# Performance work log

Hardware: AMD Instinct MI355X
Metric: run time of the kernel (lower is better)

The kernel has to match this reference:

```python
import jax, jax.numpy as jnp
import numpy as np

HEAD_NUM, HEAD_DIM, HIDDEN = 16, 64, 1024


def setup_inputs() -> dict:
    key = jax.random.key(0)
    ks = jax.random.split(key, 9)
    s = 1.0 / np.sqrt(HIDDEN)
    x = jax.random.normal(ks[0], (4, 2048, HIDDEN), dtype=jnp.float32)
    Wq = jax.random.uniform(ks[1], (HIDDEN, HIDDEN), jnp.float32, -s, s)
    bq = jax.random.uniform(ks[2], (HIDDEN,), jnp.float32, -s, s)
    Wk = jax.random.uniform(ks[3], (HIDDEN, HIDDEN), jnp.float32, -s, s)
    bk = jax.random.uniform(ks[4], (HIDDEN,), jnp.float32, -s, s)
    Wv = jax.random.uniform(ks[5], (HIDDEN, HIDDEN), jnp.float32, -s, s)
    bv = jax.random.uniform(ks[6], (HIDDEN,), jnp.float32, -s, s)
    Wo = jax.random.uniform(ks[7], (HIDDEN, HIDDEN), jnp.float32, -s, s)
    bo = jax.random.uniform(ks[8], (HIDDEN,), jnp.float32, -s, s)
    return {"x": x, "Wq": Wq, "bq": bq, "Wk": Wk, "bk": bk,
            "Wv": Wv, "bv": bv, "Wo": Wo, "bo": bo}


def reference(x, Wq, bq, Wk, bk, Wv, bv, Wo, bo):
    B, S, _ = x.shape
    H, D = HEAD_NUM, HEAD_DIM
    # Linear: x @ W^T + b (torch nn.Linear convention)
    q = (x @ Wq.T + bq).reshape(B, S, H, D).transpose(0, 2, 1, 3)  # [B,H,S,D]
    k = (x @ Wk.T + bk).reshape(B, S, H, D).transpose(0, 2, 1, 3)
    v = (x @ Wv.T + bv).reshape(B, S, H, D).transpose(0, 2, 1, 3)
    scores = jnp.einsum('bhqd,bhkd->bhqk', q, k) / np.sqrt(D)  # [B,H,S,S]
    attn = jax.nn.softmax(scores, axis=-1)  # dropout p=0.0 -> identity
    out = jnp.einsum('bhqk,bhkd->bhqd', attn, v)
    out = out.transpose(0, 2, 1, 3).reshape(B, S, H * D)
    return out @ Wo.T + bo
```

## Files before the change

### kernel.cpp

```cpp
#include <hip/hip_runtime.h>
#include <hip/hip_bf16.h>


typedef __attribute__((ext_vector_type(8))) short short8;
typedef __attribute__((ext_vector_type(4))) short short4b;
typedef __attribute__((ext_vector_type(4))) float floatx4;

#define HID 1024
#define SEQ 2048
#define BATCH 4
#define NH 16
#define HD 64
#define M_TOT (BATCH * SEQ)

#define BM 128
#define BN 128
#define BK 64

#define SCALE2 0.1803368801111204f

typedef const __attribute__((address_space(1))) void g_void;
typedef __attribute__((address_space(3))) void lds_void;

static __device__ __forceinline__ ushort f2bf(float f) {
    union { float f; unsigned int u; } v;
    v.f = f;
    unsigned int u = v.u;
    return (ushort)((u + 0x7fffu + ((u >> 16) & 1u)) >> 16);
}
static __device__ __forceinline__ ushort4 f4tobf(float4 f) {
    ushort4 r;
    r.x = f2bf(f.x); r.y = f2bf(f.y); r.z = f2bf(f.z); r.w = f2bf(f.w);
    return r;
}
static __device__ __forceinline__ unsigned int pack2bf_trunc(float lo, float hi) {
    union { float f; unsigned int u; } a, b;
    a.f = lo; b.f = hi;
    return (b.u & 0xffff0000u) | (a.u >> 16);
}

#define X_F4 (M_TOT * HID / 4)
#define W_F4 (HID * HID / 4)

__global__ __launch_bounds__(256) void convert_bf16(
    const float* __restrict__ x,
    const float* __restrict__ wq, const float* __restrict__ wk,
    const float* __restrict__ wv, const float* __restrict__ wo,
    ushort* __restrict__ xo,
    ushort* __restrict__ wqo, ushort* __restrict__ wko,
    ushort* __restrict__ wvo, ushort* __restrict__ woo)
{
    long i = (long)blockIdx.x * 256 + threadIdx.x;
    const float4* src; ushort4* dst; long off;
    if (i < X_F4)                  { src = (const float4*)x;  dst = (ushort4*)xo;  off = i; }
    else if (i < X_F4 + W_F4)      { src = (const float4*)wq; dst = (ushort4*)wqo; off = i - X_F4; }
    else if (i < X_F4 + 2 * W_F4)  { src = (const float4*)wk; dst = (ushort4*)wko; off = i - X_F4 - W_F4; }
    else if (i < X_F4 + 3 * W_F4)  { src = (const float4*)wv; dst = (ushort4*)wvo; off = i - X_F4 - 2 * W_F4; }
    else                           { src = (const float4*)wo; dst = (ushort4*)woo; off = i - X_F4 - 3 * W_F4; }
    dst[off] = f4tobf(src[off]);
}

template <int MODE>
__global__ __launch_bounds__(256) void gemm_bf(
    const ushort* __restrict__ A,
    const ushort* __restrict__ W0, const ushort* __restrict__ W1,
    const ushort* __restrict__ W2,
    const float* __restrict__ b0, const float* __restrict__ b1,
    const float* __restrict__ b2,
    ushort* __restrict__ o0, ushort* __restrict__ o1, ushort* __restrict__ o2,
    float* __restrict__ of)
{
    __shared__ ushort As[BM * BK];
    __shared__ ushort Bs[BN * BK];

    const int tid  = threadIdx.x;
    const int wave = tid >> 6;
    const int lane = tid & 63;
    const int l16  = lane & 15;
    const int lq   = lane >> 4;

    const int m0 = blockIdx.x * BM;
    const int n0 = blockIdx.y * BN;
    const int z  = (MODE == 1) ? blockIdx.z : 0;

    const ushort* W   = (z == 0) ? W0 : (z == 1) ? W1 : W2;
    const float* bias = (z == 0) ? b0 : (z == 1) ? b1 : b2;

    const int wm = (wave & 1) * 64;
    const int wn = (wave >> 1) * 64;

    const int srow = lane >> 3;
    const int schk = (lane & 7) ^ srow;
    const ushort* gA = A + (size_t)(m0 + wave * 32 + srow) * HID + schk * 8;
    const ushort* gW = W + (size_t)(n0 + wave * 32 + srow) * HID + schk * 8;
    ushort* lA = As + (wave * 32) * BK;
    ushort* lB = Bs + (wave * 32) * BK;

    floatx4 acc[4][4];
#pragma unroll
    for (int i = 0; i < 4; i++)
#pragma unroll
        for (int j = 0; j < 4; j++)
            acc[i][j] = (floatx4){0.f, 0.f, 0.f, 0.f};

    for (int k0 = 0; k0 < HID; k0 += BK) {
        __syncthreads();
#pragma unroll
        for (int i = 0; i < 4; i++) {
            __builtin_amdgcn_global_load_lds(
                (g_void*)(gA + (size_t)(8 * i) * HID + k0),
                (lds_void*)(lA + (8 * i) * BK), 16, 0, 0);
            __builtin_amdgcn_global_load_lds(
                (g_void*)(gW + (size_t)(8 * i) * HID + k0),
                (lds_void*)(lB + (8 * i) * BK), 16, 0, 0);
        }
        __syncthreads();

        const int sw = l16 & 7;
#pragma unroll
        for (int kk8 = 0; kk8 < 8; kk8 += 4) {
            short8 a[4], b[4];
#pragma unroll
            for (int i = 0; i < 4; i++)
                a[i] = *(const short8*)(&As[(wm + i * 16 + l16) * BK + ((lq + kk8) ^ sw) * 8]);
#pragma unroll
            for (int j = 0; j < 4; j++)
                b[j] = *(const short8*)(&Bs[(wn + j * 16 + l16) * BK + ((lq + kk8) ^ sw) * 8]);
#pragma unroll
            for (int i = 0; i < 4; i++)
#pragma unroll
                for (int j = 0; j < 4; j++)
                    acc[i][j] = __builtin_amdgcn_mfma_f32_16x16x32_bf16(
                        a[i], b[j], acc[i][j], 0, 0, 0);
        }
    }

    if (MODE == 0) {
#pragma unroll
        for (int j = 0; j < 4; j++) {
            int n = n0 + wn + j * 16 + l16;
            float bv = bias[n];
#pragma unroll
            for (int i = 0; i < 4; i++)
#pragma unroll
                for (int r = 0; r < 4; r++) {
                    int m = m0 + wm + i * 16 + lq * 4 + r;
                    of[(size_t)m * HID + n] = acc[i][j][r] + bv;
                }
        }
    } else if (z == 2) {
        ushort* out = o2;
#pragma unroll
        for (int j = 0; j < 4; j++) {
            int n = n0 + wn + j * 16 + l16;
            float bv = bias[n];
            int h_ = n >> 6, d_ = n & (HD - 1);
#pragma unroll
            for (int i = 0; i < 4; i++) {
                int m = m0 + wm + i * 16 + lq * 4;
                int b_ = m >> 11, s0 = m & (SEQ - 1);
                ushort4 pk;
                pk.x = f2bf(acc[i][j][0] + bv);
                pk.y = f2bf(acc[i][j][1] + bv);
                pk.z = f2bf(acc[i][j][2] + bv);
                pk.w = f2bf(acc[i][j][3] + bv);
                *(ushort4*)(out + (((size_t)b_ * NH + h_) * HD + d_) * SEQ + s0) = pk;
            }
        }
    } else {
        ushort* out = (z == 0) ? o0 : o1;
        const float sc = (z == 0) ? SCALE2 : 1.0f;
#pragma unroll
        for (int j = 0; j < 4; j++) {
            int n = n0 + wn + j * 16 + l16;
            float bv = bias[n];
            int h_ = n >> 6, d_ = n & (HD - 1);
#pragma unroll
            for (int i = 0; i < 4; i++)
#pragma unroll
                for (int r = 0; r < 4; r++) {
                    int m = m0 + wm + i * 16 + lq * 4 + r;
                    int b_ = m >> 11, s_ = m & (SEQ - 1);
                    out[(((size_t)b_ * NH + h_) * SEQ + s_) * HD + d_] =
                        f2bf((acc[i][j][r] + bv) * sc);
                }
        }
    }
}

__global__ __launch_bounds__(256) void attn_flash(
    const ushort* __restrict__ q, const ushort* __restrict__ k,
    const ushort* __restrict__ v, ushort* __restrict__ o)
{
    __shared__ ushort Ks[64 * 64];
    __shared__ ushort Vs[64 * 64];

    const int tid  = threadIdx.x;
    const int wave = tid >> 6;
    const int lane = tid & 63;
    const int l16  = lane & 15;
    const int lq   = lane >> 4;
    const int e    = l16 & 7;

    const int qb = blockIdx.x;
    const int bh = blockIdx.y;
    const int b_ = bh >> 4, h_ = bh & 15;

    const size_t base = (size_t)bh * SEQ * HD;
    const ushort* Q  = q + base;
    const ushort* K  = k + base;
    const ushort* Vt = v + base;

    const int q0 = qb * 128 + wave * 32;

    short8 qf[2][2];
#pragma unroll
    for (int f = 0; f < 2; f++) {
        const ushort* qrow = Q + (size_t)(q0 + f * 16 + l16) * HD;
        qf[f][0] = *(const short8*)(qrow + lq * 8);
        qf[f][1] = *(const short8*)(qrow + 32 + lq * 8);
    }

    const int srow = lane >> 3;
    const int schk = (lane & 7) ^ srow;
    const ushort* gK = K  + (size_t)(wave * 8 + srow) * HD  + schk * 8;
    const ushort* gV = Vt + (size_t)(wave * 8 + srow) * SEQ + schk * 8;

    floatx4 oacc[2][4];
#pragma unroll
    for (int f = 0; f < 2; f++)
#pragma unroll
        for (int jd = 0; jd < 4; jd++) oacc[f][jd] = (floatx4){0.f, 0.f, 0.f, 0.f};
    float l_[2] = {0.f, 0.f};

    const int c0 = lq ^ e;
    const int c1 = (lq + 4) ^ e;

    for (int t = 0; t < SEQ / 64; t++) {
        __syncthreads();
#pragma unroll
        for (int i = 0; i < 2; i++) {
            __builtin_amdgcn_global_load_lds(
                (g_void*)(gK + (size_t)(t * 64 + i * 32) * HD),
                (lds_void*)(Ks + (i * 32 + wave * 8) * 64), 16, 0, 0);
            __builtin_amdgcn_global_load_lds(
                (g_void*)(gV + (size_t)(i * 32) * SEQ + t * 64),
                (lds_void*)(Vs + (i * 32 + wave * 8) * 64), 16, 0, 0);
        }
        __syncthreads();

        floatx4 st[2][4];
#pragma unroll
        for (int j = 0; j < 4; j++) {
            short8 kf0 = *(const short8*)(&Ks[(j * 16 + l16) * 64 + c0 * 8]);
            short8 kf1 = *(const short8*)(&Ks[(j * 16 + l16) * 64 + c1 * 8]);
#pragma unroll
            for (int f = 0; f < 2; f++) {
                floatx4 zz = (floatx4){0.f, 0.f, 0.f, 0.f};
                zz = __builtin_amdgcn_mfma_f32_16x16x32_bf16(kf0, qf[f][0], zz, 0, 0, 0);
                st[f][j] = __builtin_amdgcn_mfma_f32_16x16x32_bf16(kf1, qf[f][1], zz, 0, 0, 0);
            }
        }

        short4b pf[2][4];
#pragma unroll
        for (int f = 0; f < 2; f++) {
            float rs = 0.f;
#pragma unroll
            for (int j = 0; j < 4; j++) {
                float p0 = __builtin_amdgcn_exp2f(st[f][j][0]);
                float p1 = __builtin_amdgcn_exp2f(st[f][j][1]);
                float p2 = __builtin_amdgcn_exp2f(st[f][j][2]);
                float p3 = __builtin_amdgcn_exp2f(st[f][j][3]);
                rs += (p0 + p1) + (p2 + p3);
                union { unsigned int u[2]; short4b s; } pk;
                pk.u[0] = pack2bf_trunc(p0, p1);
                pk.u[1] = pack2bf_trunc(p2, p3);
                pf[f][j] = pk.s;
            }
            l_[f] += rs;
        }

#pragma unroll
        for (int j = 0; j < 4; j++) {
#pragma unroll
            for (int jd = 0; jd < 4; jd++) {
                short4b vf = *(const short4b*)(
                    &Vs[(jd * 16 + l16) * 64 + ((2 * j + (lq >> 1)) ^ e) * 8 + (lq & 1) * 4]);
                oacc[0][jd] = __builtin_amdgcn_mfma_f32_16x16x16bf16_1k(
                    vf, pf[0][j], oacc[0][jd], 0, 0, 0);
                oacc[1][jd] = __builtin_amdgcn_mfma_f32_16x16x16bf16_1k(
                    vf, pf[1][j], oacc[1][jd], 0, 0, 0);
            }
        }
    }

#pragma unroll
    for (int f = 0; f < 2; f++) {
        l_[f] += __shfl_xor(l_[f], 16, 64);
        l_[f] += __shfl_xor(l_[f], 32, 64);
    }
#pragma unroll
    for (int f = 0; f < 2; f++) {
        int qg = q0 + f * 16 + l16;
        float invl = 1.0f / l_[f];
#pragma unroll
        for (int jd = 0; jd < 4; jd++) {
            ushort4 pk;
            pk.x = f2bf(oacc[f][jd][0] * invl);
            pk.y = f2bf(oacc[f][jd][1] * invl);
            pk.z = f2bf(oacc[f][jd][2] * invl);
            pk.w = f2bf(oacc[f][jd][3] * invl);
            *(ushort4*)(o + ((size_t)b_ * SEQ + qg) * HID + h_ * HD + jd * 16 + lq * 4) = pk;
        }
    }
}

extern "C" void kernel_launch(void* const* d_in, const int* in_sizes, int n_in,
                              void* d_out, int out_size, void* d_ws, size_t ws_size,
                              hipStream_t stream)
{
    const float* x  = (const float*)d_in[0];
    const float* Wq = (const float*)d_in[1];
    const float* bq = (const float*)d_in[2];
    const float* Wk = (const float*)d_in[3];
    const float* bk = (const float*)d_in[4];
    const float* Wv = (const float*)d_in[5];
    const float* bv = (const float*)d_in[6];
    const float* Wo = (const float*)d_in[7];
    const float* bo = (const float*)d_in[8];
    float* out = (float*)d_out;

    const size_t TE = (size_t)M_TOT * HID;
    const size_t WE = (size_t)HID * HID;
    ushort* qws = (ushort*)d_ws;
    ushort* kws = qws + TE;
    ushort* vws = kws + TE;
    ushort* xbf = vws + TE;
    ushort* aws = xbf;
    ushort* wqb = xbf + TE;
    ushort* wkb = wqb + WE;
    ushort* wvb = wkb + WE;
    ushort* wob = wvb + WE;

    convert_bf16<<<(X_F4 + 4 * W_F4) / 256, 256, 0, stream>>>(
        x, Wq, Wk, Wv, Wo, xbf, wqb, wkb, wvb, wob);

    dim3 g1(M_TOT / BM, HID / BN, 3);
    gemm_bf<1><<<g1, 256, 0, stream>>>(xbf, wqb, wkb, wvb, bq, bk, bv,
                                       qws, kws, vws, nullptr);

    dim3 g2(SEQ / 128, BATCH * NH, 1);
    attn_flash<<<g2, 256, 0, stream>>>(qws, kws, vws, aws);

    dim3 g3(M_TOT / BM, HID / BN, 1);
    gemm_bf<0><<<g3, 256, 0, stream>>>(aws, wob, wob, wob, bo, bo, bo,
                                       nullptr, nullptr, nullptr, out);
}
```

Before: 336.7 us.

## Halve attention query tile per block to 64 rows and use perm for bf16 packing

Each wave in the flash attention kernel now processes 16 query rows instead of 32, so a block covers 64 queries and the grid doubles along the sequence dimension. This lowers register pressure and gives more blocks for occupancy and load balance. The cost is that K/V tiles are loaded into LDS twice as often overall, which means less reuse per load. The bf16 truncating pack is also rewritten as a single v_perm byte-select instruction.

```diff
diff --git a/kernel.cpp b/kernel.cpp
--- a/kernel.cpp
+++ b/kernel.cpp
@@ -33,10 +33,8 @@
     r.x = f2bf(f.x); r.y = f2bf(f.y); r.z = f2bf(f.z); r.w = f2bf(f.w);
     return r;
 }
-static __device__ __forceinline__ unsigned int pack2bf_trunc(float lo, float hi) {
-    union { float f; unsigned int u; } a, b;
-    a.f = lo; b.f = hi;
-    return (b.u & 0xffff0000u) | (a.u >> 16);
+static __device__ __forceinline__ unsigned int fbits(float f) {
+    union { float f; unsigned int u; } v; v.f = f; return v.u;
 }
 
 #define X_F4 (M_TOT * HID / 4)
@@ -211,14 +209,13 @@
     const ushort* K  = k + base;
     const ushort* Vt = v + base;
 
-    const int q0 = qb * 128 + wave * 32;
-
-    short8 qf[2][2];
-#pragma unroll
-    for (int f = 0; f < 2; f++) {
-        const ushort* qrow = Q + (size_t)(q0 + f * 16 + l16) * HD;
-        qf[f][0] = *(const short8*)(qrow + lq * 8);
-        qf[f][1] = *(const short8*)(qrow + 32 + lq * 8);
+    const int q0 = qb * 64 + wave * 16;
+
+    short8 qf[2];
+    {
+        const ushort* qrow = Q + (size_t)(q0 + l16) * HD;
+        qf[0] = *(const short8*)(qrow + lq * 8);
+        qf[1] = *(const short8*)(qrow + 32 + lq * 8);
     }
 
     const int srow = lane >> 3;
@@ -226,12 +223,10 @@
     const ushort* gK = K  + (size_t)(wave * 8 + srow) * HD  + schk * 8;
     const ushort* gV = Vt + (size_t)(wave * 8 + srow) * SEQ + schk * 8;
 
-    floatx4 oacc[2][4];
-#pragma unroll
-    for (int f = 0; f < 2; f++)
-#pragma unroll
-        for (int jd = 0; jd < 4; jd++) oacc[f][jd] = (floatx4){0.f, 0.f, 0.f, 0.f};
-    float l_[2] = {0.f, 0.f};
+    floatx4 oacc[4];
+#pragma unroll
+    for (int jd = 0; jd < 4; jd++) oacc[jd] = (floatx4){0.f, 0.f, 0.f, 0.f};
+    float l_ = 0.f;
 
     const int c0 = lq ^ e;
     const int c1 = (lq + 4) ^ e;
@@ -249,37 +244,31 @@
         }
         __syncthreads();
 
-        floatx4 st[2][4];
+        floatx4 st[4];
 #pragma unroll
         for (int j = 0; j < 4; j++) {
             short8 kf0 = *(const short8*)(&Ks[(j * 16 + l16) * 64 + c0 * 8]);
             short8 kf1 = *(const short8*)(&Ks[(j * 16 + l16) * 64 + c1 * 8]);
-#pragma unroll
-            for (int f = 0; f < 2; f++) {
-                floatx4 zz = (floatx4){0.f, 0.f, 0.f, 0.f};
-                zz = __builtin_amdgcn_mfma_f32_16x16x32_bf16(kf0, qf[f][0], zz, 0, 0, 0);
-                st[f][j] = __builtin_amdgcn_mfma_f32_16x16x32_bf16(kf1, qf[f][1], zz, 0, 0, 0);
-            }
-        }
-
-        short4b pf[2][4];
-#pragma unroll
-        for (int f = 0; f < 2; f++) {
-            float rs = 0.f;
-#pragma unroll
-            for (int j = 0; j < 4; j++) {
-                float p0 = __builtin_amdgcn_exp2f(st[f][j][0]);
-                float p1 = __builtin_amdgcn_exp2f(st[f][j][1]);
-                float p2 = __builtin_amdgcn_exp2f(st[f][j][2]);
-                float p3 = __builtin_amdgcn_exp2f(st[f][j][3]);
-                rs += (p0 + p1) + (p2 + p3);
-                union { unsigned int u[2]; short4b s; } pk;
-                pk.u[0] = pack2bf_trunc(p0, p1);
-                pk.u[1] = pack2bf_trunc(p2, p3);
-                pf[f][j] = pk.s;
-            }
-            l_[f] += rs;
-        }
+            floatx4 zz = (floatx4){0.f, 0.f, 0.f, 0.f};
+            zz = __builtin_amdgcn_mfma_f32_16x16x32_bf16(kf0, qf[0], zz, 0, 0, 0);
+            st[j] = __builtin_amdgcn_mfma_f32_16x16x32_bf16(kf1, qf[1], zz, 0, 0, 0);
+        }
+
+        short4b pf[4];
+        float rs = 0.f;
+#pragma unroll
+        for (int j = 0; j < 4; j++) {
+            float p0 = __builtin_amdgcn_exp2f(st[j][0]);
+            float p1 = __builtin_amdgcn_exp2f(st[j][1]);
+            float p2 = __builtin_amdgcn_exp2f(st[j][2]);
+            float p3 = __builtin_amdgcn_exp2f(st[j][3]);
+            rs += (p0 + p1) + (p2 + p3);
+            union { unsigned int u[2]; short4b s; } pk;
+            pk.u[0] = __builtin_amdgcn_perm(fbits(p1), fbits(p0), 0x07060302u);
+            pk.u[1] = __builtin_amdgcn_perm(fbits(p3), fbits(p2), 0x07060302u);
+            pf[j] = pk.s;
+        }
+        l_ += rs;
 
 #pragma unroll
         for (int j = 0; j < 4; j++) {
@@ -287,30 +276,25 @@
             for (int jd = 0; jd < 4; jd++) {
                 short4b vf = *(const short4b*)(
                     &Vs[(jd * 16 + l16) * 64 + ((2 * j + (lq >> 1)) ^ e) * 8 + (lq & 1) * 4]);
-                oacc[0][jd] = __builtin_amdgcn_mfma_f32_16x16x16bf16_1k(
-                    vf, pf[0][j], oacc[0][jd], 0, 0, 0);
-                oacc[1][jd] = __builtin_amdgcn_mfma_f32_16x16x16bf16_1k(
-                    vf, pf[1][j], oacc[1][jd], 0, 0, 0);
+                oacc[jd] = __builtin_amdgcn_mfma_f32_16x16x16bf16_1k(
+                    vf, pf[j], oacc[jd], 0, 0, 0);
             }
         }
     }
 
-#pragma unroll
-    for (int f = 0; f < 2; f++) {
-        l_[f] += __shfl_xor(l_[f], 16, 64);
-        l_[f] += __shfl_xor(l_[f], 32, 64);
-    }
-#pragma unroll
-    for (int f = 0; f < 2; f++) {
-        int qg = q0 + f * 16 + l16;
-        float invl = 1.0f / l_[f];
+    l_ += __shfl_xor(l_, 16, 64);
+    l_ += __shfl_xor(l_, 32, 64);
+
+    {
+        int qg = q0 + l16;
+        float invl = 1.0f / l_;
 #pragma unroll
         for (int jd = 0; jd < 4; jd++) {
             ushort4 pk;
-            pk.x = f2bf(oacc[f][jd][0] * invl);
-            pk.y = f2bf(oacc[f][jd][1] * invl);
-            pk.z = f2bf(oacc[f][jd][2] * invl);
-            pk.w = f2bf(oacc[f][jd][3] * invl);
+            pk.x = f2bf(oacc[jd][0] * invl);
+            pk.y = f2bf(oacc[jd][1] * invl);
+            pk.z = f2bf(oacc[jd][2] * invl);
+            pk.w = f2bf(oacc[jd][3] * invl);
             *(ushort4*)(o + ((size_t)b_ * SEQ + qg) * HID + h_ * HD + jd * 16 + lq * 4) = pk;
         }
     }
@@ -350,7 +334,7 @@
     gemm_bf<1><<<g1, 256, 0, stream>>>(xbf, wqb, wkb, wvb, bq, bk, bv,
                                        qws, kws, vws, nullptr);
 
-    dim3 g2(SEQ / 128, BATCH * NH, 1);
+    dim3 g2(SEQ / 64, BATCH * NH, 1);
     attn_flash<<<g2, 256, 0, stream>>>(qws, kws, vws, aws);
 
     dim3 g3(M_TOT / BM, HID / BN, 1);
```

Measured after the change: 331.1 us. Within noise of the previous version (-1.7%).

## Double-buffer K/V tiles in flash attention and store Q transposed

Applied to the files above, without the earlier changes.

The attention kernel now keeps two K/V LDS buffers and prefetches the next 64-key tile while computing on the current one. This removes one barrier per iteration and is meant to hide global-to-LDS load latency, at the cost of doubling LDS use. The QKV projection epilogue now writes Q in a transposed layout using vectorized ushort4 stores, like V, and the attention kernel gathers Q fragments element by element from that layout. The bf16 packing of probabilities uses a byte-permute instruction, and the attention kernel gets an occupancy hint of 4 blocks per CU in its launch bounds.

```diff
diff --git a/kernel.cpp b/kernel.cpp
--- a/kernel.cpp
+++ b/kernel.cpp
@@ -33,10 +33,8 @@
     r.x = f2bf(f.x); r.y = f2bf(f.y); r.z = f2bf(f.z); r.w = f2bf(f.w);
     return r;
 }
-static __device__ __forceinline__ unsigned int pack2bf_trunc(float lo, float hi) {
-    union { float f; unsigned int u; } a, b;
-    a.f = lo; b.f = hi;
-    return (b.u & 0xffff0000u) | (a.u >> 16);
+static __device__ __forceinline__ unsigned int fbits(float f) {
+    union { float f; unsigned int u; } v; v.f = f; return v.u;
 }
 
 #define X_F4 (M_TOT * HID / 4)
@@ -148,8 +146,26 @@
                     of[(size_t)m * HID + n] = acc[i][j][r] + bv;
                 }
         }
-    } else if (z == 2) {
-        ushort* out = o2;
+    } else if (z == 1) {
+        ushort* out = o1;
+#pragma unroll
+        for (int j = 0; j < 4; j++) {
+            int n = n0 + wn + j * 16 + l16;
+            float bv = bias[n];
+            int h_ = n >> 6, d_ = n & (HD - 1);
+#pragma unroll
+            for (int i = 0; i < 4; i++)
+#pragma unroll
+                for (int r = 0; r < 4; r++) {
+                    int m = m0 + wm + i * 16 + lq * 4 + r;
+                    int b_ = m >> 11, s_ = m & (SEQ - 1);
+                    out[(((size_t)b_ * NH + h_) * SEQ + s_) * HD + d_] =
+                        f2bf(acc[i][j][r] + bv);
+                }
+        }
+    } else {
+        ushort* out = (z == 0) ? o0 : o2;
+        const float sc = (z == 0) ? SCALE2 : 1.0f;
 #pragma unroll
         for (int j = 0; j < 4; j++) {
             int n = n0 + wn + j * 16 + l16;
@@ -160,40 +176,22 @@
                 int m = m0 + wm + i * 16 + lq * 4;
                 int b_ = m >> 11, s0 = m & (SEQ - 1);
                 ushort4 pk;
-                pk.x = f2bf(acc[i][j][0] + bv);
-                pk.y = f2bf(acc[i][j][1] + bv);
-                pk.z = f2bf(acc[i][j][2] + bv);
-                pk.w = f2bf(acc[i][j][3] + bv);
+                pk.x = f2bf((acc[i][j][0] + bv) * sc);
+                pk.y = f2bf((acc[i][j][1] + bv) * sc);
+                pk.z = f2bf((acc[i][j][2] + bv) * sc);
+                pk.w = f2bf((acc[i][j][3] + bv) * sc);
                 *(ushort4*)(out + (((size_t)b_ * NH + h_) * HD + d_) * SEQ + s0) = pk;
             }
         }
-    } else {
-        ushort* out = (z == 0) ? o0 : o1;
-        const float sc = (z == 0) ? SCALE2 : 1.0f;
-#pragma unroll
-        for (int j = 0; j < 4; j++) {
-            int n = n0 + wn + j * 16 + l16;
-            float bv = bias[n];
-            int h_ = n >> 6, d_ = n & (HD - 1);
-#pragma unroll
-            for (int i = 0; i < 4; i++)
-#pragma unroll
-                for (int r = 0; r < 4; r++) {
-                    int m = m0 + wm + i * 16 + lq * 4 + r;
-                    int b_ = m >> 11, s_ = m & (SEQ - 1);
-                    out[(((size_t)b_ * NH + h_) * SEQ + s_) * HD + d_] =
-                        f2bf((acc[i][j][r] + bv) * sc);
-                }
-        }
-    }
-}
-
-__global__ __launch_bounds__(256) void attn_flash(
+    }
+}
+
+__global__ __launch_bounds__(256, 4) void attn_flash(
     const ushort* __restrict__ q, const ushort* __restrict__ k,
     const ushort* __restrict__ v, ushort* __restrict__ o)
 {
-    __shared__ ushort Ks[64 * 64];
-    __shared__ ushort Vs[64 * 64];
+    __shared__ ushort Ks[2 * 64 * 64];
+    __shared__ ushort Vs[2 * 64 * 64];
 
     const int tid  = threadIdx.x;
     const int wave = tid >> 6;
@@ -207,7 +205,7 @@
     const int b_ = bh >> 4, h_ = bh & 15;
 
     const size_t base = (size_t)bh * SEQ * HD;
-    const ushort* Q  = q + base;
+    const ushort* Qt = q + base;
     const ushort* K  = k + base;
     const ushort* Vt = v + base;
 
@@ -215,11 +213,12 @@
 
     short8 qf[2][2];
 #pragma unroll
-    for (int f = 0; f < 2; f++) {
-        const ushort* qrow = Q + (size_t)(q0 + f * 16 + l16) * HD;
-        qf[f][0] = *(const short8*)(qrow + lq * 8);
-        qf[f][1] = *(const short8*)(qrow + 32 + lq * 8);
-    }
+    for (int f = 0; f < 2; f++)
+#pragma unroll
+        for (int jj = 0; jj < 8; jj++) {
+            qf[f][0][jj] = (short)Qt[(size_t)(lq * 8 + jj) * SEQ + q0 + f * 16 + l16];
+            qf[f][1][jj] = (short)Qt[(size_t)(32 + lq * 8 + jj) * SEQ + q0 + f * 16 + l16];
+        }
 
     const int srow = lane >> 3;
     const int schk = (lane & 7) ^ srow;
@@ -236,24 +235,40 @@
     const int c0 = lq ^ e;
     const int c1 = (lq + 4) ^ e;
 
+#pragma unroll
+    for (int i = 0; i < 2; i++) {
+        __builtin_amdgcn_global_load_lds(
+            (g_void*)(gK + (size_t)(i * 32) * HD),
+            (lds_void*)(Ks + (i * 32 + wave * 8) * 64), 16, 0, 0);
+        __builtin_amdgcn_global_load_lds(
+            (g_void*)(gV + (size_t)(i * 32) * SEQ),
+            (lds_void*)(Vs + (i * 32 + wave * 8) * 64), 16, 0, 0);
+    }
+
     for (int t = 0; t < SEQ / 64; t++) {
         __syncthreads();
-#pragma unroll
-        for (int i = 0; i < 2; i++) {
-            __builtin_amdgcn_global_load_lds(
-                (g_void*)(gK + (size_t)(t * 64 + i * 32) * HD),
-                (lds_void*)(Ks + (i * 32 + wave * 8) * 64), 16, 0, 0);
-            __builtin_amdgcn_global_load_lds(
-                (g_void*)(gV + (size_t)(i * 32) * SEQ + t * 64),
-                (lds_void*)(Vs + (i * 32 + wave * 8) * 64), 16, 0, 0);
-        }
-        __syncthreads();
+
+        if (t + 1 < SEQ / 64) {
+            const int nb = (t + 1) & 1;
+#pragma unroll
+            for (int i = 0; i < 2; i++) {
+                __builtin_amdgcn_global_load_lds(
+                    (g_void*)(gK + (size_t)((t + 1) * 64 + i * 32) * HD),
+                    (lds_void*)(Ks + nb * 4096 + (i * 32 + wave * 8) * 64), 16, 0, 0);
+                __builtin_amdgcn_global_load_lds(
+                    (g_void*)(gV + (size_t)(i * 32) * SEQ + (t + 1) * 64),
+                    (lds_void*)(Vs + nb * 4096 + (i * 32 + wave * 8) * 64), 16, 0, 0);
+            }
+        }
+
+        const ushort* Kb = Ks + (t & 1) * 4096;
+        const ushort* Vb = Vs + (t & 1) * 4096;
 
         floatx4 st[2][4];
 #pragma unroll
         for (int j = 0; j < 4; j++) {
-            short8 kf0 = *(const short8*)(&Ks[(j * 16 + l16) * 64 + c0 * 8]);
-            short8 kf1 = *(const short8*)(&Ks[(j * 16 + l16) * 64 + c1 * 8]);
+            short8 kf0 = *(const short8*)(&Kb[(j * 16 + l16) * 64 + c0 * 8]);
+            short8 kf1 = *(const short8*)(&Kb[(j * 16 + l16) * 64 + c1 * 8]);
 #pragma unroll
             for (int f = 0; f < 2; f++) {
                 floatx4 zz = (floatx4){0.f, 0.f, 0.f, 0.f};
@@ -274,8 +289,8 @@
                 float p3 = __builtin_amdgcn_exp2f(st[f][j][3]);
                 rs += (p0 + p1) + (p2 + p3);
                 union { unsigned int u[2]; short4b s; } pk;
-                pk.u[0] = pack2bf_trunc(p0, p1);
-                pk.u[1] = pack2bf_trunc(p2, p3);
+                pk.u[0] = __builtin_amdgcn_perm(fbits(p1), fbits(p0), 0x07060302u);
+                pk.u[1] = __builtin_amdgcn_perm(fbits(p3), fbits(p2), 0x07060302u);
                 pf[f][j] = pk.s;
             }
             l_[f] += rs;
@@ -286,7 +301,7 @@
 #pragma unroll
             for (int jd = 0; jd < 4; jd++) {
                 short4b vf = *(const short4b*)(
-                    &Vs[(jd * 16 + l16) * 64 + ((2 * j + (lq >> 1)) ^ e) * 8 + (lq & 1) * 4]);
+                    &Vb[(jd * 16 + l16) * 64 + ((2 * j + (lq >> 1)) ^ e) * 8 + (lq & 1) * 4]);
                 oacc[0][jd] = __builtin_amdgcn_mfma_f32_16x16x16bf16_1k(
                     vf, pf[0][j], oacc[0][jd], 0, 0, 0);
                 oacc[1][jd] = __builtin_amdgcn_mfma_f32_16x16x16bf16_1k(
@@ -300,6 +315,7 @@
         l_[f] += __shfl_xor(l_[f], 16, 64);
         l_[f] += __shfl_xor(l_[f], 32, 64);
     }
+
 #pragma unroll
     for (int f = 0; f < 2; f++) {
         int qg = q0 + f * 16 + l16;
```

Measured after the change: 273.2 us. 1.23x faster.
